# Performance work log

Measured on AMD Instinct MI355X. Metric: run time of the kernel, lower is better.

## Reference

```python
import jax, jax.numpy as jnp
import numpy as np

TEMP = 0.1      # temperature
REG = 0.1       # ot_reg
MAX_ITER = 100  # Sinkhorn-style scaling iterations (original early-stops on tol; fixed-point is identical post-convergence)

B, D, N_PER = 64, 128, 512  # examples, embed dim, nodes/tokens per example


def _normalize(x):
    # torch F.normalize(dim=1): x / max(||x||, eps)
    n = jnp.linalg.norm(x, axis=1, keepdims=True)
    return x / jnp.maximum(n, 1e-12)


def setup_inputs() -> dict:
    key = jax.random.key(0)
    k0, k1, k2, k3 = jax.random.split(key, 4)
    N = B * N_PER
    return {
        "struct_global": jax.random.normal(k0, (B, D), jnp.float32),
        "seq_global": jax.random.normal(k1, (B, D), jnp.float32),
        "struct_nodes": jax.random.normal(k2, (N, D), jnp.float32),
        "seq_tokens": jax.random.normal(k3, (N, D), jnp.float32),
        # sorted, equal-size segments: example i owns rows [i*N_PER, (i+1)*N_PER)
        "batch_idx": jnp.repeat(jnp.arange(B), N_PER),
    }


def _global_nt_xent(struct_emb, seq_emb):
    s = _normalize(struct_emb)
    q = _normalize(seq_emb)
    sim = (s @ q.T) / TEMP                      # [B, B]
    loss_i = -jnp.mean(jnp.diagonal(jax.nn.log_softmax(sim, axis=1)))
    loss_j = -jnp.mean(jnp.diagonal(jax.nn.log_softmax(sim.T, axis=1)))
    return (loss_i + loss_j) / 2.0


def _local_ot_loss(struct_nodes, seq_tokens):
    # batch_idx is sorted equal-size segments -> dense batched reshape
    sn = _normalize(struct_nodes).reshape(B, N_PER, D)
    st = _normalize(seq_tokens).reshape(B, N_PER, D)
    C = -jnp.einsum('bnd,bmd->bnm', sn, st)     # [B, n, m] cost
    n = m = N_PER
    # Original detaches cost to numpy before OT -> transport plan P is a constant w.r.t. grads
    C_sg = jax.lax.stop_gradient(C)
    P0 = jnp.exp(-C_sg / REG)
    a = jnp.full((B, n), 1.0 / n, C.dtype)
    b = jnp.full((B, m), 1.0 / m, C.dtype)

    def body(_, uv):
        u, v = uv
        # Jacobi-style update: both use the previous (u, v), matching the source
        u_new = a / jnp.einsum('bnm,bm->bn', P0, v)
        v_new = b / jnp.einsum('bnm,bn->bm', P0, u)
        u_new = jnp.nan_to_num(u_new, nan=1.0 / n, posinf=1.0 / n, neginf=1.0 / n)
        v_new = jnp.nan_to_num(v_new, nan=1.0 / m, posinf=1.0 / m, neginf=1.0 / m)
        return (u_new, v_new)

    u, v = jax.lax.fori_loop(0, MAX_ITER, body, (a, b))  # init u=1/n, v=1/m as in source
    P = u[:, :, None] * P0 * v[:, None, :]      # diag(u) @ P0 @ diag(v)
    total = jnp.sum(P * C)                      # grads flow through C only
    return total / B


def reference(struct_global, seq_global, struct_nodes, seq_tokens, batch_idx):
    global_loss = _global_nt_xent(struct_global, seq_global)
    local_loss = _local_ot_loss(struct_nodes, seq_tokens)
    total_loss = global_loss + local_loss
    return (global_loss, local_loss, total_loss)
```

## Files before the change

### kernel.cpp

```cpp
#include <hip/hip_runtime.h>
#include <cstdint>
#include <cmath>

#define NB_EX 64
#define DIMD 128
#define NP 512
constexpr float MARG = 1.0f / 512.0f;

__device__ __forceinline__ float bf2f_lo(unsigned w) { return __uint_as_float(w << 16); }
__device__ __forceinline__ float bf2f_hi(unsigned w) { return __uint_as_float(w & 0xFFFF0000u); }
__device__ __forceinline__ unsigned short f2bf(float f) {
    unsigned u = __float_as_uint(f);
    u += 0x7FFFu + ((u >> 16) & 1u);
    return (unsigned short)(u >> 16);
}
__device__ __forceinline__ float wred64(float v) {
#pragma unroll
    for (int m = 1; m < 64; m <<= 1) v += __shfl_xor(v, m, 64);
    return v;
}

__device__ __forceinline__ void wg_barrier_lds() {
    __builtin_amdgcn_sched_barrier(0);
    asm volatile("s_waitcnt lgkmcnt(0)\n\ts_barrier" ::: "memory");
    __builtin_amdgcn_sched_barrier(0);
}

__device__ __forceinline__ int self_detect(const unsigned* probe, int t) {
    __shared__ int sd_cnt[4];
    unsigned w = probe[t];
    unsigned e = (w >> 7) & 0xFFu;
    unsigned long long m = __ballot(e >= 110u && e <= 130u);
    if ((t & 63) == 0) sd_cnt[t >> 6] = __popcll(m);
    __syncthreads();
    int c = sd_cnt[0] + sd_cnt[1] + sd_cnt[2] + sd_cnt[3];
    __syncthreads();
    return c >= 128;
}

#define O_SIMG   0
#define O_RNAN   16384
#define O_RNBN   147456
#define O_COLP   278528
#define O_COLPIF 2375680
#define O_P0     4472832

__global__ void k_rnormAB(const void* anr, const void* bnr, float* rnan, float* rnbn) {
    int t = threadIdx.x;
    int flag = self_detect((const unsigned*)anr, t);
    int gr  = blockIdx.x * 4 + (t >> 6);
    int lane = t & 63;
    const void* in = (gr < 32768) ? anr : bnr;
    float* rn      = (gr < 32768) ? rnan : rnbn;
    int row = gr & 32767;
    float f0, f1;
    if (flag) {
        unsigned w = ((const unsigned*)in)[row * 64 + lane];
        f0 = bf2f_lo(w); f1 = bf2f_hi(w);
    } else {
        float2 v = ((const float2*)in)[row * 64 + lane];
        f0 = v.x; f1 = v.y;
    }
    float ss = wred64(f0 * f0 + f1 * f1);
    if (lane == 0) rn[row] = 1.0f / fmaxf(sqrtf(ss), 1e-12f);
}

__global__ void k_simg(const void* sgr, const void* qgr, float* simg) {
    __shared__ float rls[128];
    int t = threadIdx.x;
    int flag = self_detect((const unsigned*)sgr, t);
    int w = t >> 6, lane = t & 63;
    for (int rr = 0; rr < 32; rr++) {
        int ri = w * 32 + rr;
        const void* base = (ri < 64) ? sgr : qgr;
        int row = ri & 63;
        float f0, f1;
        if (flag) {
            unsigned wd = ((const unsigned*)base)[row * 64 + lane];
            f0 = bf2f_lo(wd); f1 = bf2f_hi(wd);
        } else {
            float2 v = ((const float2*)base)[row * 64 + lane];
            f0 = v.x; f1 = v.y;
        }
        float ss = wred64(f0 * f0 + f1 * f1);
        if (lane == 0) rls[ri] = 1.0f / fmaxf(sqrtf(ss), 1e-12f);
    }
    __syncthreads();
    int g = blockIdx.x * 256 + t;
    int i = g >> 6, j = g & 63;
    float dot = 0.f;
    if (flag) {
        const unsigned* a = (const unsigned*)sgr + i * 64;
        const unsigned* b = (const unsigned*)qgr + j * 64;
        for (int k = 0; k < 64; k++) {
            unsigned wa = a[k], wb = b[k];
            dot += bf2f_lo(wa) * bf2f_lo(wb);
            dot += bf2f_hi(wa) * bf2f_hi(wb);
        }
    } else {
        const float4* a = (const float4*)sgr + i * 32;
        const float4* b = (const float4*)qgr + j * 32;
        for (int k = 0; k < 32; k++) {
            float4 x = a[k], y = b[k];
            dot += x.x * y.x + x.y * y.y + x.z * y.z + x.w * y.w;
        }
    }
    simg[g] = dot * rls[i] * rls[64 + j] * 10.0f;
}

__global__ void k_gloss(const float* __restrict__ simg, float* outf) {
    __shared__ float red[64];
    int i = threadIdx.x;
    if (i < 64) {
        float m = -1e30f;
        for (int j = 0; j < 64; j++) m = fmaxf(m, simg[i * 64 + j]);
        float se = 0.f;
        for (int j = 0; j < 64; j++) se += expf(simg[i * 64 + j] - m);
        float rl = simg[i * 64 + i] - (m + logf(se));
        float m2 = -1e30f;
        for (int j = 0; j < 64; j++) m2 = fmaxf(m2, simg[j * 64 + i]);
        float se2 = 0.f;
        for (int j = 0; j < 64; j++) se2 += expf(simg[j * 64 + i] - m2);
        float cl = simg[i * 64 + i] - (m2 + logf(se2));
        red[i] = rl + cl;
    }
    __syncthreads();
    if (i == 0) {
        float s = 0.f;
        for (int k = 0; k < 64; k++) s += red[k];
        float g = -s / 128.0f;
        outf[0] = g;
        outf[1] = 0.0f;
        outf[2] = g;
    }
}

__global__ void k_build(const void* anr, const void* bnr, const float* rnan, const float* rnbn,
                        unsigned short* p0) {
    int t  = threadIdx.x;
    int flag = self_detect((const unsigned*)anr, t);
    int b   = blockIdx.y;
    int r0t = (blockIdx.x >> 2) * 128;
    int c0t = (blockIdx.x & 3) * 128;
    __shared__ float As[128][33];
    __shared__ float Bs[128][33];
    int tr = t >> 4, tc = t & 15;
    float acc[8][8];
#pragma unroll
    for (int i = 0; i < 8; i++)
#pragma unroll
        for (int j = 0; j < 8; j++) acc[i][j] = 0.f;

    for (int kc = 0; kc < 4; kc++) {
        for (int ii = 0; ii < 4; ii++) {
            int idx = t + 256 * ii;
            int r = idx >> 3, c4 = idx & 7;
            {
                int grow = b * NP + r0t + r;
                float sc = rnan[grow];
                float f0, f1, f2, f3;
                if (flag) {
                    const unsigned* src = (const unsigned*)anr + ((grow * DIMD + kc * 32 + c4 * 4) >> 1);
                    unsigned w0 = src[0], w1 = src[1];
                    f0 = bf2f_lo(w0); f1 = bf2f_hi(w0); f2 = bf2f_lo(w1); f3 = bf2f_hi(w1);
                } else {
                    float4 v = *((const float4*)((const float*)anr + grow * DIMD + kc * 32 + c4 * 4));
                    f0 = v.x; f1 = v.y; f2 = v.z; f3 = v.w;
                }
                As[r][c4 * 4 + 0] = f0 * sc; As[r][c4 * 4 + 1] = f1 * sc;
                As[r][c4 * 4 + 2] = f2 * sc; As[r][c4 * 4 + 3] = f3 * sc;
            }
            {
                int grow = b * NP + c0t + r;
                float sc = rnbn[grow];
                float f0, f1, f2, f3;
                if (flag) {
                    const unsigned* src = (const unsigned*)bnr + ((grow * DIMD + kc * 32 + c4 * 4) >> 1);
                    unsigned w0 = src[0], w1 = src[1];
                    f0 = bf2f_lo(w0); f1 = bf2f_hi(w0); f2 = bf2f_lo(w1); f3 = bf2f_hi(w1);
                } else {
                    float4 v = *((const float4*)((const float*)bnr + grow * DIMD + kc * 32 + c4 * 4));
                    f0 = v.x; f1 = v.y; f2 = v.z; f3 = v.w;
                }
                Bs[r][c4 * 4 + 0] = f0 * sc; Bs[r][c4 * 4 + 1] = f1 * sc;
                Bs[r][c4 * 4 + 2] = f2 * sc; Bs[r][c4 * 4 + 3] = f3 * sc;
            }
        }
        __syncthreads();
        for (int kk = 0; kk < 32; kk++) {
            float av[8], bv[8];
#pragma unroll
            for (int i = 0; i < 8; i++) av[i] = As[tr * 8 + i][kk];
#pragma unroll
            for (int j = 0; j < 8; j++) bv[j] = Bs[tc * 8 + j][kk];
#pragma unroll
            for (int i = 0; i < 8; i++)
#pragma unroll
                for (int j = 0; j < 8; j++) acc[i][j] += av[i] * bv[j];
        }
        __syncthreads();
    }
#pragma unroll
    for (int i = 0; i < 8; i++) {
        int grow = b * NP + r0t + tr * 8 + i;
        unsigned short h[8];
#pragma unroll
        for (int j = 0; j < 8; j++) h[j] = f2bf(expf(acc[i][j] * 10.0f));
        uint4 pk;
        pk.x = (unsigned)h[0] | ((unsigned)h[1] << 16);
        pk.y = (unsigned)h[2] | ((unsigned)h[3] << 16);
        pk.z = (unsigned)h[4] | ((unsigned)h[5] << 16);
        pk.w = (unsigned)h[6] | ((unsigned)h[7] << 16);
        *((uint4*)(p0 + ((size_t)grow * NP + c0t + tc * 8))) = pk;
    }
}

__device__ __forceinline__ void store_dual(unsigned* l2p, unsigned* ifp, unsigned v) {
    *l2p = v;
    __hip_atomic_store(ifp, v, __ATOMIC_RELAXED, __HIP_MEMORY_SCOPE_AGENT);
}

__device__ __forceinline__ void poll_sums(const unsigned* crdL2, const unsigned* crdIF,
                                          unsigned tag, int t, float& r0, float& r1) {
    unsigned voff = (unsigned)(t * 4) + 4096u;
    unsigned q0, q1, q2, q3, q4, q5, q6, q7;
    for (int round = 0;; ++round) {
        asm volatile(
            "global_load_dword %0, %8, %9 offset:-4096 sc0\n\t"
            "global_load_dword %1, %8, %9 offset:-2048 sc0\n\t"
            "global_load_dword %2, %8, %9 offset:0 sc0\n\t"
            "global_load_dword %3, %8, %9 offset:2048 sc0\n\t"
            "global_load_dword %4, %8, %9 offset:-3072 sc0\n\t"
            "global_load_dword %5, %8, %9 offset:-1024 sc0\n\t"
            "global_load_dword %6, %8, %9 offset:1024 sc0\n\t"
            "global_load_dword %7, %8, %9 offset:3072 sc0\n\t"
            "s_waitcnt vmcnt(0)"
            : "=&v"(q0), "=&v"(q1), "=&v"(q2), "=&v"(q3),
              "=&v"(q4), "=&v"(q5), "=&v"(q6), "=&v"(q7)
            : "v"(voff), "s"(crdL2)
            : "memory");
        if (round >= 2) {
            const unsigned* pp = crdIF + t;
            unsigned b0 = __hip_atomic_load(pp +    0, __ATOMIC_RELAXED, __HIP_MEMORY_SCOPE_AGENT);
            unsigned b1 = __hip_atomic_load(pp +  512, __ATOMIC_RELAXED, __HIP_MEMORY_SCOPE_AGENT);
            unsigned b2 = __hip_atomic_load(pp + 1024, __ATOMIC_RELAXED, __HIP_MEMORY_SCOPE_AGENT);
            unsigned b3 = __hip_atomic_load(pp + 1536, __ATOMIC_RELAXED, __HIP_MEMORY_SCOPE_AGENT);
            unsigned b4 = __hip_atomic_load(pp +  256, __ATOMIC_RELAXED, __HIP_MEMORY_SCOPE_AGENT);
            unsigned b5 = __hip_atomic_load(pp +  768, __ATOMIC_RELAXED, __HIP_MEMORY_SCOPE_AGENT);
            unsigned b6 = __hip_atomic_load(pp + 1280, __ATOMIC_RELAXED, __HIP_MEMORY_SCOPE_AGENT);
            unsigned b7 = __hip_atomic_load(pp + 1792, __ATOMIC_RELAXED, __HIP_MEMORY_SCOPE_AGENT);
            if ((q0 & 0xFFFFu) != tag) q0 = b0;
            if ((q1 & 0xFFFFu) != tag) q1 = b1;
            if ((q2 & 0xFFFFu) != tag) q2 = b2;
            if ((q3 & 0xFFFFu) != tag) q3 = b3;
            if ((q4 & 0xFFFFu) != tag) q4 = b4;
            if ((q5 & 0xFFFFu) != tag) q5 = b5;
            if ((q6 & 0xFFFFu) != tag) q6 = b6;
            if ((q7 & 0xFFFFu) != tag) q7 = b7;
        }
        bool ok = ((q0 & 0xFFFFu) == tag) && ((q1 & 0xFFFFu) == tag)
               && ((q2 & 0xFFFFu) == tag) && ((q3 & 0xFFFFu) == tag)
               && ((q4 & 0xFFFFu) == tag) && ((q5 & 0xFFFFu) == tag)
               && ((q6 & 0xFFFFu) == tag) && ((q7 & 0xFFFFu) == tag);
        if (ok) break;
        if (round >= 2) __builtin_amdgcn_s_sleep(1);
    }
    r0 = __uint_as_float(q0 & 0xFFFF0000u) + __uint_as_float(q1 & 0xFFFF0000u)
       + __uint_as_float(q2 & 0xFFFF0000u) + __uint_as_float(q3 & 0xFFFF0000u);
    r1 = __uint_as_float(q4 & 0xFFFF0000u) + __uint_as_float(q5 & 0xFFFF0000u)
       + __uint_as_float(q6 & 0xFFFF0000u) + __uint_as_float(q7 & 0xFFFF0000u);
}

__global__ __launch_bounds__(256, 1) void k_persist(const unsigned short* __restrict__ p0,
                                                    unsigned* __restrict__ colpL2,
                                                    unsigned* __restrict__ colpIF,
                                                    float* __restrict__ outf) {
    int blk = blockIdx.x;
    int rb  = blk >> 6;
    int b   = blk & 63;
    int rowbase = rb * 128;
    int t = threadIdx.x, w = t >> 6, lane = t & 63;

    __shared__ float credU[4][512];
    __shared__ float credV[4][512];
    __shared__ float v_sU[512];
    __shared__ float v_sV[512];
    __shared__ float u_sU[128];
    __shared__ float u_sV[128];
    __shared__ float bs[4];

    uint4 pw[32];
#pragma unroll
    for (int r = 0; r < 32; r++) {
        int row = rowbase + w * 32 + r;
        pw[r] = ((const uint4*)(p0 + (((size_t)(b << 9) + row) << 9)))[lane];
    }
    int col0 = t, col1 = t + 256;
    if (t < 128) u_sU[t] = MARG;
    v_sV[col0] = MARG; v_sV[col1] = MARG;
    __syncthreads();

#pragma unroll 1
    for (int s = 0; s < 50; ++s) {
        unsigned tag = (unsigned)(s + 1);
        int bank = s & 1;
        {
            float ca[8];
#pragma unroll
            for (int k = 0; k < 8; ++k) ca[k] = 0.f;
#pragma unroll
            for (int r = 0; r < 32; ++r) {
                float u_r = u_sU[w * 32 + r];
                uint4 pv = pw[r];
                ca[0] += bf2f_lo(pv.x) * u_r; ca[1] += bf2f_hi(pv.x) * u_r;
                ca[2] += bf2f_lo(pv.y) * u_r; ca[3] += bf2f_hi(pv.y) * u_r;
                ca[4] += bf2f_lo(pv.z) * u_r; ca[5] += bf2f_hi(pv.z) * u_r;
                ca[6] += bf2f_lo(pv.w) * u_r; ca[7] += bf2f_hi(pv.w) * u_r;
            }
#pragma unroll
            for (int k = 0; k < 8; ++k) credU[w][lane * 8 + k] = ca[k];
        }
        wg_barrier_lds();
        {
            int slot = ((bank * 64 + b) * 4 + rb) << 9;
            float s0 = credU[0][col0] + credU[1][col0] + credU[2][col0] + credU[3][col0];
            float s1 = credU[0][col1] + credU[1][col1] + credU[2][col1] + credU[3][col1];
            store_dual(colpL2 + slot + col0, colpIF + slot + col0,
                       ((unsigned)f2bf(s0) << 16) | tag);
            store_dual(colpL2 + slot + col1, colpIF + slot + col1,
                       ((unsigned)f2bf(s1) << 16) | tag);
        }
        {
            float vr[8];
#pragma unroll
            for (int k = 0; k < 8; ++k) vr[k] = v_sV[lane * 8 + k];
#pragma unroll
            for (int g = 0; g < 4; ++g) {
                float rp[8];
#pragma unroll
                for (int j = 0; j < 8; ++j) {
                    uint4 pv = pw[g * 8 + j];
                    rp[j] = bf2f_lo(pv.x) * vr[0] + bf2f_hi(pv.x) * vr[1]
                          + bf2f_lo(pv.y) * vr[2] + bf2f_hi(pv.y) * vr[3]
                          + bf2f_lo(pv.z) * vr[4] + bf2f_hi(pv.z) * vr[5]
                          + bf2f_lo(pv.w) * vr[6] + bf2f_hi(pv.w) * vr[7];
                }
#pragma unroll
                for (int m = 1; m < 64; m <<= 1)
#pragma unroll
                    for (int j = 0; j < 8; ++j) rp[j] += __shfl_xor(rp[j], m, 64);
                float sel = rp[0];
#pragma unroll
                for (int j = 1; j < 8; ++j) if (lane == j) sel = rp[j];
                if (lane < 8) {
                    float q = MARG / sel;
                    if (!isfinite(q)) q = MARG;
                    u_sV[w * 32 + g * 8 + lane] = q;
                }
            }
        }
        {
            float ca[8];
#pragma unroll
            for (int k = 0; k < 8; ++k) ca[k] = 0.f;
#pragma unroll
            for (int r = 0; r < 32; ++r) {
                float u_r = u_sV[w * 32 + r];
                uint4 pv = pw[r];
                ca[0] += bf2f_lo(pv.x) * u_r; ca[1] += bf2f_hi(pv.x) * u_r;
                ca[2] += bf2f_lo(pv.y) * u_r; ca[3] += bf2f_hi(pv.y) * u_r;
                ca[4] += bf2f_lo(pv.z) * u_r; ca[5] += bf2f_hi(pv.z) * u_r;
                ca[6] += bf2f_lo(pv.w) * u_r; ca[7] += bf2f_hi(pv.w) * u_r;
            }
#pragma unroll
            for (int k = 0; k < 8; ++k) credV[w][lane * 8 + k] = ca[k];
        }
        {
            int base = ((bank * 64 + b) * 4) << 9;
            float r0, r1;
            poll_sums(colpL2 + base, colpIF + base, tag, t, r0, r1);
            float q0 = MARG / r0; if (!isfinite(q0)) q0 = MARG;
            float q1 = MARG / r1; if (!isfinite(q1)) q1 = MARG;
            v_sU[col0] = q0;
            v_sU[col1] = q1;
        }
        wg_barrier_lds();
        {
            int slot = (((2 + bank) * 64 + b) * 4 + rb) << 9;
            float s0 = credV[0][col0] + credV[1][col0] + credV[2][col0] + credV[3][col0];
            float s1 = credV[0][col1] + credV[1][col1] + credV[2][col1] + credV[3][col1];
            store_dual(colpL2 + slot + col0, colpIF + slot + col0,
                       ((unsigned)f2bf(s0) << 16) | tag);
            store_dual(colpL2 + slot + col1, colpIF + slot + col1,
                       ((unsigned)f2bf(s1) << 16) | tag);
        }
        {
            float vr[8];
#pragma unroll
            for (int k = 0; k < 8; ++k) vr[k] = v_sU[lane * 8 + k];
#pragma unroll
            for (int g = 0; g < 4; ++g) {
                float rp[8];
#pragma unroll
                for (int j = 0; j < 8; ++j) {
                    uint4 pv = pw[g * 8 + j];
                    rp[j] = bf2f_lo(pv.x) * vr[0] + bf2f_hi(pv.x) * vr[1]
                          + bf2f_lo(pv.y) * vr[2] + bf2f_hi(pv.y) * vr[3]
                          + bf2f_lo(pv.z) * vr[4] + bf2f_hi(pv.z) * vr[5]
                          + bf2f_lo(pv.w) * vr[6] + bf2f_hi(pv.w) * vr[7];
                }
#pragma unroll
                for (int m = 1; m < 64; m <<= 1)
#pragma unroll
                    for (int j = 0; j < 8; ++j) rp[j] += __shfl_xor(rp[j], m, 64);
                float sel = rp[0];
#pragma unroll
                for (int j = 1; j < 8; ++j) if (lane == j) sel = rp[j];
                if (lane < 8) {
                    float q = MARG / sel;
                    if (!isfinite(q)) q = MARG;
                    u_sU[w * 32 + g * 8 + lane] = q;
                }
            }
        }
        {
            int base = (((2 + bank) * 64 + b) * 4) << 9;
            float r0, r1;
            poll_sums(colpL2 + base, colpIF + base, tag, t, r0, r1);
            float q0 = MARG / r0; if (!isfinite(q0)) q0 = MARG;
            float q1 = MARG / r1; if (!isfinite(q1)) q1 = MARG;
            v_sV[col0] = q0;
            v_sV[col1] = q1;
        }
    }
    wg_barrier_lds();

    float vr[8];
#pragma unroll
    for (int k = 0; k < 8; ++k) vr[k] = v_sV[lane * 8 + k];
    float acc = 0.f;
#pragma unroll
    for (int r = 0; r < 32; ++r) {
        float u_r = u_sU[w * 32 + r];
        uint4 pv = pw[r];
        float f[8];
        f[0] = bf2f_lo(pv.x); f[1] = bf2f_hi(pv.x);
        f[2] = bf2f_lo(pv.y); f[3] = bf2f_hi(pv.y);
        f[4] = bf2f_lo(pv.z); f[5] = bf2f_hi(pv.z);
        f[6] = bf2f_lo(pv.w); f[7] = bf2f_hi(pv.w);
#pragma unroll
        for (int k = 0; k < 8; ++k) {
            float p = f[k];
            acc += u_r * p * vr[k] * (-0.1f) * logf(p);
        }
    }
    acc = wred64(acc);
    if (lane == 0) bs[w] = acc;
    __syncthreads();
    if (t == 0) {
        float c = (bs[0] + bs[1] + bs[2] + bs[3]) * (1.0f / 64.0f);
        atomicAdd(&outf[1], c);
        atomicAdd(&outf[2], c);
    }
}

extern "C" void kernel_launch(void* const* d_in, const int* in_sizes, int n_in,
                              void* d_out, int out_size, void* d_ws, size_t ws_size,
                              hipStream_t stream) {
    const void* sg = d_in[0];
    const void* qg = d_in[1];
    const void* an = d_in[2];
    const void* bn = d_in[3];
    char* ws = (char*)d_ws;
    float* outf = (float*)d_out;

    float* simg      = (float*)(ws + O_SIMG);
    float* rnan      = (float*)(ws + O_RNAN);
    float* rnbn      = (float*)(ws + O_RNBN);
    unsigned* colpL2 = (unsigned*)(ws + O_COLP);
    unsigned* colpIF = (unsigned*)(ws + O_COLPIF);
    unsigned short* p0 = (unsigned short*)(ws + O_P0);

    k_rnormAB<<<16384, 256, 0, stream>>>(an, bn, rnan, rnbn);
    k_simg<<<16, 256, 0, stream>>>(sg, qg, simg);
    k_gloss<<<1, 256, 0, stream>>>(simg, outf);
    k_build<<<dim3(16, 64), 256, 0, stream>>>(an, bn, rnan, rnbn, p0);
    k_persist<<<256, 256, 0, stream>>>(p0, colpL2, colpIF, outf);
}
```

Baseline: 639.7 us.

## Split persistent Sinkhorn kernel across 8 row blocks per example

Adds a k_persist8 variant that gives each example 8 workgroups of 64 rows instead of 4 of 128, launching 512 persistent blocks. The aim is to use more CUs and halve the per-block register-resident P0 slice and per-iteration compute. In exchange, each column-sum poll must gather 8 partials instead of 4, which adds global traffic and cross-block sync latency per iteration. The new path runs only when the workspace is large enough; otherwise the old 4-block kernel is used. It also relies on all 512 blocks being co-resident.

```diff
diff --git a/kernel.cpp b/kernel.cpp
--- a/kernel.cpp
+++ b/kernel.cpp
@@ -44,6 +44,10 @@
 #define O_COLP   278528
 #define O_COLPIF 2375680
 #define O_P0     4472832
+#define O8_COLP   278528
+#define O8_COLPIF 8667136
+#define O8_P0     17055744
+#define NEED8     50610176ull
 
 __global__ void k_rnormAB(const void* anr, const void* bnr, float* rnan, float* rnbn) {
     int t = threadIdx.x;
@@ -220,8 +224,8 @@
     __hip_atomic_store(ifp, v, __ATOMIC_RELAXED, __HIP_MEMORY_SCOPE_AGENT);
 }
 
-__device__ __forceinline__ void poll_sums(const unsigned* crdL2, const unsigned* crdIF,
-                                          unsigned tag, int t, float& r0, float& r1) {
+__device__ __forceinline__ void poll_sums4(const unsigned* crdL2, const unsigned* crdIF,
+                                           unsigned tag, int t, float& r0, float& r1) {
     unsigned voff = (unsigned)(t * 4) + 4096u;
     unsigned q0, q1, q2, q3, q4, q5, q6, q7;
     for (int round = 0;; ++round) {
@@ -271,10 +275,64 @@
        + __uint_as_float(q6 & 0xFFFF0000u) + __uint_as_float(q7 & 0xFFFF0000u);
 }
 
-__global__ __launch_bounds__(256, 1) void k_persist(const unsigned short* __restrict__ p0,
-                                                    unsigned* __restrict__ colpL2,
-                                                    unsigned* __restrict__ colpIF,
-                                                    float* __restrict__ outf) {
+__device__ __forceinline__ void poll_sums8(const unsigned* crdL2, const unsigned* crdIF,
+                                           unsigned tag, int t, float& r0, float& r1) {
+    unsigned voffA = (unsigned)(t * 4) + 4096u;
+    unsigned voffB = voffA + 8192u;
+    unsigned q[16];
+    for (int round = 0;; ++round) {
+        asm volatile(
+            "global_load_dword %0, %16, %18 offset:-4096 sc0\n\t"
+            "global_load_dword %1, %16, %18 offset:-3072 sc0\n\t"
+            "global_load_dword %2, %16, %18 offset:-2048 sc0\n\t"
+            "global_load_dword %3, %16, %18 offset:-1024 sc0\n\t"
+            "global_load_dword %4, %16, %18 offset:0 sc0\n\t"
+            "global_load_dword %5, %16, %18 offset:1024 sc0\n\t"
+            "global_load_dword %6, %16, %18 offset:2048 sc0\n\t"
+            "global_load_dword %7, %16, %18 offset:3072 sc0\n\t"
+            "global_load_dword %8, %17, %18 offset:-4096 sc0\n\t"
+            "global_load_dword %9, %17, %18 offset:-3072 sc0\n\t"
+            "global_load_dword %10, %17, %18 offset:-2048 sc0\n\t"
+            "global_load_dword %11, %17, %18 offset:-1024 sc0\n\t"
+            "global_load_dword %12, %17, %18 offset:0 sc0\n\t"
+            "global_load_dword %13, %17, %18 offset:1024 sc0\n\t"
+            "global_load_dword %14, %17, %18 offset:2048 sc0\n\t"
+            "global_load_dword %15, %17, %18 offset:3072 sc0\n\t"
+            "s_waitcnt vmcnt(0)"
+            : "=&v"(q[0]), "=&v"(q[1]), "=&v"(q[2]), "=&v"(q[3]),
+              "=&v"(q[4]), "=&v"(q[5]), "=&v"(q[6]), "=&v"(q[7]),
+              "=&v"(q[8]), "=&v"(q[9]), "=&v"(q[10]), "=&v"(q[11]),
+              "=&v"(q[12]), "=&v"(q[13]), "=&v"(q[14]), "=&v"(q[15])
+            : "v"(voffA), "v"(voffB), "s"(crdL2)
+            : "memory");
+        if (round >= 2) {
+            const unsigned* pp = crdIF + t;
+#pragma unroll
+            for (int p = 0; p < 8; ++p) {
+                unsigned bc0 = __hip_atomic_load(pp + p * 512,       __ATOMIC_RELAXED, __HIP_MEMORY_SCOPE_AGENT);
+                unsigned bc1 = __hip_atomic_load(pp + p * 512 + 256, __ATOMIC_RELAXED, __HIP_MEMORY_SCOPE_AGENT);
+                if ((q[2 * p]     & 0xFFFFu) != tag) q[2 * p]     = bc0;
+                if ((q[2 * p + 1] & 0xFFFFu) != tag) q[2 * p + 1] = bc1;
+            }
+        }
+        bool ok = true;
+#pragma unroll
+        for (int k = 0; k < 16; ++k) ok = ok && ((q[k] & 0xFFFFu) == tag);
+        if (ok) break;
+        if (round >= 2) __builtin_amdgcn_s_sleep(1);
+    }
+    r0 = 0.f; r1 = 0.f;
+#pragma unroll
+    for (int p = 0; p < 8; ++p) {
+        r0 += __uint_as_float(q[2 * p]     & 0xFFFF0000u);
+        r1 += __uint_as_float(q[2 * p + 1] & 0xFFFF0000u);
+    }
+}
+
+__global__ __launch_bounds__(256, 1) void k_persist4(const unsigned short* __restrict__ p0,
+                                                     unsigned* __restrict__ colpL2,
+                                                     unsigned* __restrict__ colpIF,
+                                                     float* __restrict__ outf) {
     int blk = blockIdx.x;
     int rb  = blk >> 6;
     int b   = blk & 63;
@@ -378,7 +436,7 @@
         {
             int base = ((bank * 64 + b) * 4) << 9;
             float r0, r1;
-            poll_sums(colpL2 + base, colpIF + base, tag, t, r0, r1);
+            poll_sums4(colpL2 + base, colpIF + base, tag, t, r0, r1);
             float q0 = MARG / r0; if (!isfinite(q0)) q0 = MARG;
             float q1 = MARG / r1; if (!isfinite(q1)) q1 = MARG;
             v_sU[col0] = q0;
@@ -426,7 +484,7 @@
         {
             int base = (((2 + bank) * 64 + b) * 4) << 9;
             float r0, r1;
-            poll_sums(colpL2 + base, colpIF + base, tag, t, r0, r1);
+            poll_sums4(colpL2 + base, colpIF + base, tag, t, r0, r1);
             float q0 = MARG / r0; if (!isfinite(q0)) q0 = MARG;
             float q1 = MARG / r1; if (!isfinite(q1)) q1 = MARG;
             v_sV[col0] = q0;
@@ -442,6 +500,199 @@
 #pragma unroll
     for (int r = 0; r < 32; ++r) {
         float u_r = u_sU[w * 32 + r];
+        uint4 pv = pw[r];
+        float f[8];
+        f[0] = bf2f_lo(pv.x); f[1] = bf2f_hi(pv.x);
+        f[2] = bf2f_lo(pv.y); f[3] = bf2f_hi(pv.y);
+        f[4] = bf2f_lo(pv.z); f[5] = bf2f_hi(pv.z);
+        f[6] = bf2f_lo(pv.w); f[7] = bf2f_hi(pv.w);
+#pragma unroll
+        for (int k = 0; k < 8; ++k) {
+            float p = f[k];
+            acc += u_r * p * vr[k] * (-0.1f) * logf(p);
+        }
+    }
+    acc = wred64(acc);
+    if (lane == 0) bs[w] = acc;
+    __syncthreads();
+    if (t == 0) {
+        float c = (bs[0] + bs[1] + bs[2] + bs[3]) * (1.0f / 64.0f);
+        atomicAdd(&outf[1], c);
+        atomicAdd(&outf[2], c);
+    }
+}
+
+__global__ void k_persist8(const unsigned short* __restrict__ p0,
+                           unsigned* __restrict__ colpL2,
+                           unsigned* __restrict__ colpIF,
+                           float* __restrict__ outf) {
+    int blk = blockIdx.x;
+    int rb  = blk >> 6;
+    int b   = blk & 63;
+    int rowbase = rb * 64;
+    int t = threadIdx.x, w = t >> 6, lane = t & 63;
+
+    __shared__ float credU[4][512];
+    __shared__ float credV[4][512];
+    __shared__ float v_sU[512];
+    __shared__ float v_sV[512];
+    __shared__ float u_sU[64];
+    __shared__ float u_sV[64];
+    __shared__ float bs[4];
+
+    uint4 pw[16];
+#pragma unroll
+    for (int r = 0; r < 16; r++) {
+        int row = rowbase + w * 16 + r;
+        pw[r] = ((const uint4*)(p0 + (((size_t)(b << 9) + row) << 9)))[lane];
+    }
+    int col0 = t, col1 = t + 256;
+    if (t < 64) u_sU[t] = MARG;
+    v_sV[col0] = MARG; v_sV[col1] = MARG;
+    __syncthreads();
+
+#pragma unroll 1
+    for (int s = 0; s < 50; ++s) {
+        unsigned tag = (unsigned)(s + 1);
+        int bank = s & 1;
+        {
+            float ca[8];
+#pragma unroll
+            for (int k = 0; k < 8; ++k) ca[k] = 0.f;
+#pragma unroll
+            for (int r = 0; r < 16; ++r) {
+                float u_r = u_sU[w * 16 + r];
+                uint4 pv = pw[r];
+                ca[0] += bf2f_lo(pv.x) * u_r; ca[1] += bf2f_hi(pv.x) * u_r;
+                ca[2] += bf2f_lo(pv.y) * u_r; ca[3] += bf2f_hi(pv.y) * u_r;
+                ca[4] += bf2f_lo(pv.z) * u_r; ca[5] += bf2f_hi(pv.z) * u_r;
+                ca[6] += bf2f_lo(pv.w) * u_r; ca[7] += bf2f_hi(pv.w) * u_r;
+            }
+#pragma unroll
+            for (int k = 0; k < 8; ++k) credU[w][lane * 8 + k] = ca[k];
+        }
+        wg_barrier_lds();
+        {
+            int slot = ((bank * 64 + b) * 8 + rb) << 9;
+            float s0 = credU[0][col0] + credU[1][col0] + credU[2][col0] + credU[3][col0];
+            float s1 = credU[0][col1] + credU[1][col1] + credU[2][col1] + credU[3][col1];
+            store_dual(colpL2 + slot + col0, colpIF + slot + col0,
+                       ((unsigned)f2bf(s0) << 16) | tag);
+            store_dual(colpL2 + slot + col1, colpIF + slot + col1,
+                       ((unsigned)f2bf(s1) << 16) | tag);
+        }
+        {
+            float vr[8];
+#pragma unroll
+            for (int k = 0; k < 8; ++k) vr[k] = v_sV[lane * 8 + k];
+#pragma unroll
+            for (int g = 0; g < 2; ++g) {
+                float rp[8];
+#pragma unroll
+                for (int j = 0; j < 8; ++j) {
+                    uint4 pv = pw[g * 8 + j];
+                    rp[j] = bf2f_lo(pv.x) * vr[0] + bf2f_hi(pv.x) * vr[1]
+                          + bf2f_lo(pv.y) * vr[2] + bf2f_hi(pv.y) * vr[3]
+                          + bf2f_lo(pv.z) * vr[4] + bf2f_hi(pv.z) * vr[5]
+                          + bf2f_lo(pv.w) * vr[6] + bf2f_hi(pv.w) * vr[7];
+                }
+#pragma unroll
+                for (int m = 1; m < 64; m <<= 1)
+#pragma unroll
+                    for (int j = 0; j < 8; ++j) rp[j] += __shfl_xor(rp[j], m, 64);
+                float sel = rp[0];
+#pragma unroll
+                for (int j = 1; j < 8; ++j) if (lane == j) sel = rp[j];
+                if (lane < 8) {
+                    float q = MARG / sel;
+                    if (!isfinite(q)) q = MARG;
+                    u_sV[w * 16 + g * 8 + lane] = q;
+                }
+            }
+        }
+        {
+            float ca[8];
+#pragma unroll
+            for (int k = 0; k < 8; ++k) ca[k] = 0.f;
+#pragma unroll
+            for (int r = 0; r < 16; ++r) {
+                float u_r = u_sV[w * 16 + r];
+                uint4 pv = pw[r];
+                ca[0] += bf2f_lo(pv.x) * u_r; ca[1] += bf2f_hi(pv.x) * u_r;
+                ca[2] += bf2f_lo(pv.y) * u_r; ca[3] += bf2f_hi(pv.y) * u_r;
+                ca[4] += bf2f_lo(pv.z) * u_r; ca[5] += bf2f_hi(pv.z) * u_r;
+                ca[6] += bf2f_lo(pv.w) * u_r; ca[7] += bf2f_hi(pv.w) * u_r;
+            }
+#pragma unroll
+            for (int k = 0; k < 8; ++k) credV[w][lane * 8 + k] = ca[k];
+        }
+        {
+            int base = ((bank * 64 + b) * 8) << 9;
+            float r0, r1;
+            poll_sums8(colpL2 + base, colpIF + base, tag, t, r0, r1);
+            float q0 = MARG / r0; if (!isfinite(q0)) q0 = MARG;
+            float q1 = MARG / r1; if (!isfinite(q1)) q1 = MARG;
+            v_sU[col0] = q0;
+            v_sU[col1] = q1;
+        }
+        wg_barrier_lds();
+        {
+            int slot = (((2 + bank) * 64 + b) * 8 + rb) << 9;
+            float s0 = credV[0][col0] + credV[1][col0] + credV[2][col0] + credV[3][col0];
+            float s1 = credV[0][col1] + credV[1][col1] + credV[2][col1] + credV[3][col1];
+            store_dual(colpL2 + slot + col0, colpIF + slot + col0,
+                       ((unsigned)f2bf(s0) << 16) | tag);
+            store_dual(colpL2 + slot + col1, colpIF + slot + col1,
+                       ((unsigned)f2bf(s1) << 16) | tag);
+        }
+        {
+            float vr[8];
+#pragma unroll
+            for (int k = 0; k < 8; ++k) vr[k] = v_sU[lane * 8 + k];
+#pragma unroll
+            for (int g = 0; g < 2; ++g) {
+                float rp[8];
+#pragma unroll
+                for (int j = 0; j < 8; ++j) {
+                    uint4 pv = pw[g * 8 + j];
+                    rp[j] = bf2f_lo(pv.x) * vr[0] + bf2f_hi(pv.x) * vr[1]
+                          + bf2f_lo(pv.y) * vr[2] + bf2f_hi(pv.y) * vr[3]
+                          + bf2f_lo(pv.z) * vr[4] + bf2f_hi(pv.z) * vr[5]
+                          + bf2f_lo(pv.w) * vr[6] + bf2f_hi(pv.w) * vr[7];
+                }
+#pragma unroll
+                for (int m = 1; m < 64; m <<= 1)
+#pragma unroll
+                    for (int j = 0; j < 8; ++j) rp[j] += __shfl_xor(rp[j], m, 64);
+                float sel = rp[0];
+#pragma unroll
+                for (int j = 1; j < 8; ++j) if (lane == j) sel = rp[j];
+                if (lane < 8) {
+                    float q = MARG / sel;
+                    if (!isfinite(q)) q = MARG;
+                    u_sU[w * 16 + g * 8 + lane] = q;
+                }
+            }
+        }
+        {
+            int base = (((2 + bank) * 64 + b) * 8) << 9;
+            float r0, r1;
+            poll_sums8(colpL2 + base, colpIF + base, tag, t, r0, r1);
+            float q0 = MARG / r0; if (!isfinite(q0)) q0 = MARG;
+            float q1 = MARG / r1; if (!isfinite(q1)) q1 = MARG;
+            v_sV[col0] = q0;
+            v_sV[col1] = q1;
+        }
+    }
+    wg_barrier_lds();
+
+    float vr[8];
+#pragma unroll
+    for (int k = 0; k < 8; ++k) vr[k] = v_sV[lane * 8 + k];
+    float acc = 0.f;
+#pragma unroll
+    for (int r = 0; r < 16; ++r) {
+        float u_r = u_sU[w * 16 + r];
         uint4 pv = pw[r];
         float f[8];
         f[0] = bf2f_lo(pv.x); f[1] = bf2f_hi(pv.x);
@@ -474,16 +725,25 @@
     char* ws = (char*)d_ws;
     float* outf = (float*)d_out;
 
-    float* simg      = (float*)(ws + O_SIMG);
-    float* rnan      = (float*)(ws + O_RNAN);
-    float* rnbn      = (float*)(ws + O_RNBN);
-    unsigned* colpL2 = (unsigned*)(ws + O_COLP);
-    unsigned* colpIF = (unsigned*)(ws + O_COLPIF);
-    unsigned short* p0 = (unsigned short*)(ws + O_P0);
+    float* simg = (float*)(ws + O_SIMG);
+    float* rnan = (float*)(ws + O_RNAN);
+    float* rnbn = (float*)(ws + O_RNBN);
 
     k_rnormAB<<<16384, 256, 0, stream>>>(an, bn, rnan, rnbn);
     k_simg<<<16, 256, 0, stream>>>(sg, qg, simg);
     k_gloss<<<1, 256, 0, stream>>>(simg, outf);
-    k_build<<<dim3(16, 64), 256, 0, stream>>>(an, bn, rnan, rnbn, p0);
-    k_persist<<<256, 256, 0, stream>>>(p0, colpL2, colpIF, outf);
-}
+
+    if (ws_size >= NEED8) {
+        unsigned* colpL2 = (unsigned*)(ws + O8_COLP);
+        unsigned* colpIF = (unsigned*)(ws + O8_COLPIF);
+        unsigned short* p0 = (unsigned short*)(ws + O8_P0);
+        k_build<<<dim3(16, 64), 256, 0, stream>>>(an, bn, rnan, rnbn, p0);
+        k_persist8<<<512, 256, 0, stream>>>(p0, colpL2, colpIF, outf);
+    } else {
+        unsigned* colpL2 = (unsigned*)(ws + O_COLP);
+        unsigned* colpIF = (unsigned*)(ws + O_COLPIF);
+        unsigned short* p0 = (unsigned short*)(ws + O_P0);
+        k_build<<<dim3(16, 64), 256, 0, stream>>>(an, bn, rnan, rnbn, p0);
+        k_persist4<<<256, 256, 0, stream>>>(p0, colpL2, colpIF, outf);
+    }
+}
```

Measured after the change: 1.694 ms. 165% more time.

## Fuse row-norm computation into build kernel and merge global-loss kernels

Applied to the files above, without the earlier changes.

Removes the standalone row-norm kernel by having each build block compute inverse norms for its 128 A rows and 128 B rows into shared memory before the GEMM. It also merges the global similarity and NT-Xent loss kernels into one single-block kernel that keeps the similarity matrix in LDS. This cuts three launches and a global round-trip for the norms. In exchange, norms are recomputed four times per row across blocks, and the global-loss work now runs on a single block instead of sixteen.

```diff
diff --git a/kernel.cpp b/kernel.cpp
--- a/kernel.cpp
+++ b/kernel.cpp
@@ -45,28 +45,10 @@
 #define O_COLPIF 2375680
 #define O_P0     4472832
 
-__global__ void k_rnormAB(const void* anr, const void* bnr, float* rnan, float* rnbn) {
-    int t = threadIdx.x;
-    int flag = self_detect((const unsigned*)anr, t);
-    int gr  = blockIdx.x * 4 + (t >> 6);
-    int lane = t & 63;
-    const void* in = (gr < 32768) ? anr : bnr;
-    float* rn      = (gr < 32768) ? rnan : rnbn;
-    int row = gr & 32767;
-    float f0, f1;
-    if (flag) {
-        unsigned w = ((const unsigned*)in)[row * 64 + lane];
-        f0 = bf2f_lo(w); f1 = bf2f_hi(w);
-    } else {
-        float2 v = ((const float2*)in)[row * 64 + lane];
-        f0 = v.x; f1 = v.y;
-    }
-    float ss = wred64(f0 * f0 + f1 * f1);
-    if (lane == 0) rn[row] = 1.0f / fmaxf(sqrtf(ss), 1e-12f);
-}
-
-__global__ void k_simg(const void* sgr, const void* qgr, float* simg) {
+__global__ void k_global(const void* sgr, const void* qgr, float* outf) {
     __shared__ float rls[128];
+    __shared__ float simg_s[4096];
+    __shared__ float red[64];
     int t = threadIdx.x;
     int flag = self_detect((const unsigned*)sgr, t);
     int w = t >> 6, lane = t & 63;
@@ -86,42 +68,41 @@
         if (lane == 0) rls[ri] = 1.0f / fmaxf(sqrtf(ss), 1e-12f);
     }
     __syncthreads();
-    int g = blockIdx.x * 256 + t;
-    int i = g >> 6, j = g & 63;
-    float dot = 0.f;
-    if (flag) {
-        const unsigned* a = (const unsigned*)sgr + i * 64;
-        const unsigned* b = (const unsigned*)qgr + j * 64;
-        for (int k = 0; k < 64; k++) {
-            unsigned wa = a[k], wb = b[k];
-            dot += bf2f_lo(wa) * bf2f_lo(wb);
-            dot += bf2f_hi(wa) * bf2f_hi(wb);
-        }
-    } else {
-        const float4* a = (const float4*)sgr + i * 32;
-        const float4* b = (const float4*)qgr + j * 32;
-        for (int k = 0; k < 32; k++) {
-            float4 x = a[k], y = b[k];
-            dot += x.x * y.x + x.y * y.y + x.z * y.z + x.w * y.w;
-        }
-    }
-    simg[g] = dot * rls[i] * rls[64 + j] * 10.0f;
-}
-
-__global__ void k_gloss(const float* __restrict__ simg, float* outf) {
-    __shared__ float red[64];
-    int i = threadIdx.x;
+    for (int n = 0; n < 16; n++) {
+        int g = n * 256 + t;
+        int i = g >> 6, j = g & 63;
+        float dot = 0.f;
+        if (flag) {
+            const unsigned* a = (const unsigned*)sgr + i * 64;
+            const unsigned* b = (const unsigned*)qgr + j * 64;
+            for (int k = 0; k < 64; k++) {
+                unsigned wa = a[k], wb = b[k];
+                dot += bf2f_lo(wa) * bf2f_lo(wb);
+                dot += bf2f_hi(wa) * bf2f_hi(wb);
+            }
+        } else {
+            const float4* a = (const float4*)sgr + i * 32;
+            const float4* b = (const float4*)qgr + j * 32;
+            for (int k = 0; k < 32; k++) {
+                float4 x = a[k], y = b[k];
+                dot += x.x * y.x + x.y * y.y + x.z * y.z + x.w * y.w;
+            }
+        }
+        simg_s[g] = dot * rls[i] * rls[64 + j] * 10.0f;
+    }
+    __syncthreads();
+    int i = t;
     if (i < 64) {
         float m = -1e30f;
-        for (int j = 0; j < 64; j++) m = fmaxf(m, simg[i * 64 + j]);
+        for (int j = 0; j < 64; j++) m = fmaxf(m, simg_s[i * 64 + j]);
         float se = 0.f;
-        for (int j = 0; j < 64; j++) se += expf(simg[i * 64 + j] - m);
-        float rl = simg[i * 64 + i] - (m + logf(se));
+        for (int j = 0; j < 64; j++) se += expf(simg_s[i * 64 + j] - m);
+        float rl = simg_s[i * 64 + i] - (m + logf(se));
         float m2 = -1e30f;
-        for (int j = 0; j < 64; j++) m2 = fmaxf(m2, simg[j * 64 + i]);
+        for (int j = 0; j < 64; j++) m2 = fmaxf(m2, simg_s[j * 64 + i]);
         float se2 = 0.f;
-        for (int j = 0; j < 64; j++) se2 += expf(simg[j * 64 + i] - m2);
-        float cl = simg[i * 64 + i] - (m2 + logf(se2));
+        for (int j = 0; j < 64; j++) se2 += expf(simg_s[j * 64 + i] - m2);
+        float cl = simg_s[i * 64 + i] - (m2 + logf(se2));
         red[i] = rl + cl;
     }
     __syncthreads();
@@ -135,8 +116,7 @@
     }
 }
 
-__global__ void k_build(const void* anr, const void* bnr, const float* rnan, const float* rnbn,
-                        unsigned short* p0) {
+__global__ void k_build2(const void* anr, const void* bnr, unsigned short* p0) {
     int t  = threadIdx.x;
     int flag = self_detect((const unsigned*)anr, t);
     int b   = blockIdx.y;
@@ -144,6 +124,30 @@
     int c0t = (blockIdx.x & 3) * 128;
     __shared__ float As[128][33];
     __shared__ float Bs[128][33];
+    __shared__ float rnA[128];
+    __shared__ float rnB[128];
+    int w = t >> 6, lane = t & 63;
+    for (int rr = 0; rr < 64; ++rr) {
+        int ri = w * 64 + rr;
+        int isA = (ri < 128);
+        int grow = isA ? (b * NP + r0t + ri) : (b * NP + c0t + (ri - 128));
+        const void* in = isA ? anr : bnr;
+        float f0, f1;
+        if (flag) {
+            unsigned wd = ((const unsigned*)in)[grow * 64 + lane];
+            f0 = bf2f_lo(wd); f1 = bf2f_hi(wd);
+        } else {
+            float2 v = ((const float2*)in)[grow * 64 + lane];
+            f0 = v.x; f1 = v.y;
+        }
+        float ss = wred64(f0 * f0 + f1 * f1);
+        if (lane == 0) {
+            float rn = 1.0f / fmaxf(sqrtf(ss), 1e-12f);
+            if (isA) rnA[ri] = rn; else rnB[ri - 128] = rn;
+        }
+    }
+    __syncthreads();
+
     int tr = t >> 4, tc = t & 15;
     float acc[8][8];
 #pragma unroll
@@ -157,7 +161,7 @@
             int r = idx >> 3, c4 = idx & 7;
             {
                 int grow = b * NP + r0t + r;
-                float sc = rnan[grow];
+                float sc = rnA[r];
                 float f0, f1, f2, f3;
                 if (flag) {
                     const unsigned* src = (const unsigned*)anr + ((grow * DIMD + kc * 32 + c4 * 4) >> 1);
@@ -172,7 +176,7 @@
             }
             {
                 int grow = b * NP + c0t + r;
-                float sc = rnbn[grow];
+                float sc = rnB[r];
                 float f0, f1, f2, f3;
                 if (flag) {
                     const unsigned* src = (const unsigned*)bnr + ((grow * DIMD + kc * 32 + c4 * 4) >> 1);
@@ -474,16 +478,11 @@
     char* ws = (char*)d_ws;
     float* outf = (float*)d_out;
 
-    float* simg      = (float*)(ws + O_SIMG);
-    float* rnan      = (float*)(ws + O_RNAN);
-    float* rnbn      = (float*)(ws + O_RNBN);
     unsigned* colpL2 = (unsigned*)(ws + O_COLP);
     unsigned* colpIF = (unsigned*)(ws + O_COLPIF);
     unsigned short* p0 = (unsigned short*)(ws + O_P0);
 
-    k_rnormAB<<<16384, 256, 0, stream>>>(an, bn, rnan, rnbn);
-    k_simg<<<16, 256, 0, stream>>>(sg, qg, simg);
-    k_gloss<<<1, 256, 0, stream>>>(simg, outf);
-    k_build<<<dim3(16, 64), 256, 0, stream>>>(an, bn, rnan, rnbn, p0);
+    k_build2<<<dim3(16, 64), 256, 0, stream>>>(an, bn, p0);
+    k_global<<<1, 256, 0, stream>>>(sg, qg, outf);
     k_persist<<<256, 256, 0, stream>>>(p0, colpL2, colpIF, outf);
 }
```

After: 712.9 us. 11.4% more time.
